# Performance work log

Hardware: AMD Instinct MI355X
Metric: run time of the kernel (lower is better)

Reference implementation:

```python
import jax, jax.numpy as jnp
import numpy as np

D_MODEL = 512
NUM_HEADS = 8
NUM_REL_EMB = 1024


def _linear(x, w, b):
    # torch nn.Linear convention: w is [out, in]
    return x @ w.T + b


def setup_inputs() -> dict:
    key = jax.random.key(0)
    B, S, D = 1, 512, D_MODEL
    ks = jax.random.split(key, 14)
    scale = D ** -0.5
    def w(i):
        return jax.random.normal(ks[i], (D, D), jnp.float32) * scale
    def b(i):
        return jax.random.normal(ks[i], (D,), jnp.float32) * 0.01
    return {
        "hidden_states": jax.random.normal(ks[0], (B, S, D), jnp.float32),
        "emb_table": jax.random.normal(ks[1], (NUM_REL_EMB, D), jnp.float32) * 0.02,
        "wq": w(2), "bq": b(3),
        "wk": w(4), "bk": b(5),
        "wv": w(6), "bv": b(7),
        "wrk": w(8), "brk": b(9),
        "wrq": w(10), "brq": b(11),
        "wo": w(12), "bo": b(13),
    }


def reference(hidden_states, emb_table, wq, bq, wk, bk, wv, bv,
              wrk, brk, wrq, brq, wo, bo):
    B, S, D = hidden_states.shape
    H = NUM_HEADS
    hd = D // H
    NE = emb_table.shape[0]

    # relative positions j - i, shifted and clamped, then embedded: [S, S, D]
    rel_pos = jnp.arange(S)[None, :] - jnp.arange(S)[:, None]
    idx = jnp.clip(rel_pos + NE // 2, 0, NE - 1)
    rel_emb = emb_table[idx]  # [S, S, D] (identical across batch)

    q = _linear(hidden_states, wq, bq).reshape(B, S, H, hd).transpose(0, 2, 1, 3)  # [B,H,S,hd]
    k = _linear(hidden_states, wk, bk).reshape(B, S, H, hd).transpose(0, 2, 1, 3)
    v = _linear(hidden_states, wv, bv).reshape(B, S, H, hd).transpose(0, 2, 1, 3)

    rk = _linear(rel_emb, wrk, brk).reshape(S, S, H, hd)  # [i, j, H, hd]
    rq = _linear(rel_emb, wrq, brq).reshape(S, S, H, hd)

    # content-content + content-relative + relative-content scores: [B,H,S,S]
    scores = (
        jnp.einsum('bhid,bhjd->bhij', q, k)
        + jnp.einsum('bhid,ijhd->bhij', q, rk)
        + jnp.einsum('ijhd,bhjd->bhij', rq, k)
    )

    attn = jax.nn.softmax(scores / jnp.sqrt(jnp.asarray(hd, scores.dtype)), axis=-1)
    # dropout is identity (p=0.0 / eval mode)

    ctx = jnp.einsum('bhij,bhjd->bhid', attn, v)          # [B,H,S,hd]
    ctx = ctx.transpose(0, 2, 1, 3).reshape(B, S, D)       # merge heads
    out = _linear(ctx, wo, bo)
    return out, attn
```

## Files before the change

kernel.cpp:

```cpp
#include <hip/hip_runtime.h>
#include <stdint.h>


typedef __bf16 bf16_t;
typedef bf16_t bf16x8 __attribute__((ext_vector_type(8)));
typedef float f32x4 __attribute__((ext_vector_type(4)));

__device__ __forceinline__ uint16_t f2bf(float f) {
  union { float f; uint32_t i; } c; c.f = f;
  return (uint16_t)((c.i + 0x7fffu + ((c.i >> 16) & 1u)) >> 16);
}
__device__ __forceinline__ uint32_t pack2bf(float lo, float hi) {
  return (uint32_t)f2bf(lo) | ((uint32_t)f2bf(hi) << 16);
}
#define MFMA(a, b, c) __builtin_amdgcn_mfma_f32_16x16x32_bf16((a), (b), (c), 0, 0, 0)

#define LSTR 40
#define SSTR 72

__global__ __launch_bounds__(256) void gemm_bt_kernel(
    const void* __restrict__ A, int lda, int zsA, int aF32,
    const void* __restrict__ B, int ldb, int zsB, int bF32,
    const float* __restrict__ bias, int hasBias,
    float* __restrict__ C, int ldc, int zsC, int K)
{
  __shared__ __align__(16) uint16_t As[64 * LSTR];
  __shared__ __align__(16) uint16_t Bs[64 * LSTR];
  const int z = blockIdx.z;
  const int m0 = blockIdx.y * 64, n0 = blockIdx.x * 64;
  const int t = threadIdx.x, lane = t & 63, wave = t >> 6;
  const int wi = wave & 1, wj = wave >> 1;
  const int quad = lane >> 4, l15 = lane & 15;
  const int srow = t >> 2, scol = (t & 3) * 8;

  f32x4 acc[2][2] = {};
  for (int k0 = 0; k0 < K; k0 += 32) {
    uint4 ap, bp;
    if (aF32) {
      const float* Af = (const float*)A + (size_t)z * zsA + (size_t)(m0 + srow) * lda + (k0 + scol);
      float4 x0 = *(const float4*)(Af); float4 x1 = *(const float4*)(Af + 4);
      ap.x = pack2bf(x0.x, x0.y); ap.y = pack2bf(x0.z, x0.w);
      ap.z = pack2bf(x1.x, x1.y); ap.w = pack2bf(x1.z, x1.w);
    } else {
      ap = *(const uint4*)((const uint16_t*)A + (size_t)z * zsA + (size_t)(m0 + srow) * lda + (k0 + scol));
    }
    if (bF32) {
      const float* Bf = (const float*)B + (size_t)z * zsB + (size_t)(n0 + srow) * ldb + (k0 + scol);
      float4 x0 = *(const float4*)(Bf); float4 x1 = *(const float4*)(Bf + 4);
      bp.x = pack2bf(x0.x, x0.y); bp.y = pack2bf(x0.z, x0.w);
      bp.z = pack2bf(x1.x, x1.y); bp.w = pack2bf(x1.z, x1.w);
    } else {
      bp = *(const uint4*)((const uint16_t*)B + (size_t)z * zsB + (size_t)(n0 + srow) * ldb + (k0 + scol));
    }
    *(uint4*)(&As[srow * LSTR + scol]) = ap;
    *(uint4*)(&Bs[srow * LSTR + scol]) = bp;
    __syncthreads();
    bf16x8 af[2], bfr[2];
#pragma unroll
    for (int x = 0; x < 2; x++) {
      af[x]  = *(const bf16x8*)(&As[(wi * 32 + x * 16 + l15) * LSTR + quad * 8]);
      bfr[x] = *(const bf16x8*)(&Bs[(wj * 32 + x * 16 + l15) * LSTR + quad * 8]);
    }
#pragma unroll
    for (int x = 0; x < 2; x++)
#pragma unroll
      for (int y = 0; y < 2; y++)
        acc[x][y] = MFMA(af[x], bfr[y], acc[x][y]);
    __syncthreads();
  }
#pragma unroll
  for (int x = 0; x < 2; x++)
#pragma unroll
    for (int y = 0; y < 2; y++) {
      const int j = n0 + wj * 32 + y * 16 + l15;
      const float bval = hasBias ? bias[j] : 0.0f;
      const int ib = m0 + wi * 32 + x * 16 + quad * 4;
#pragma unroll
      for (int r = 0; r < 4; r++)
        C[(size_t)z * zsC + (size_t)(ib + r) * ldc + j] = acc[x][y][r] + bval;
    }
}

__global__ __launch_bounds__(256) void proj_kernel(
    const float* __restrict__ X, const float* __restrict__ emb,
    const float* __restrict__ wq, const float* __restrict__ bq,
    const float* __restrict__ wk, const float* __restrict__ bk,
    const float* __restrict__ wv, const float* __restrict__ bv,
    const float* __restrict__ wrk, const float* __restrict__ brk,
    const float* __restrict__ wrq, const float* __restrict__ brq,
    uint16_t* __restrict__ q, uint16_t* __restrict__ k, uint16_t* __restrict__ vT,
    uint16_t* __restrict__ rkE, uint16_t* __restrict__ rqE)
{
  int bid = blockIdx.x;
  const float *A, *B, *bias; uint16_t* C; int mode;
  if (bid < 64)       {            A = X;   B = wq;  bias = bq;  C = q;   mode = 2; }
  else if (bid < 128) { bid -= 64; A = X;   B = wk;  bias = bk;  C = k;   mode = 2; }
  else if (bid < 192) { bid -= 128; A = X;  B = wv;  bias = bv;  C = vT;  mode = 3; }
  else if (bid < 320) { bid -= 192; A = emb; B = wrk; bias = brk; C = rkE; mode = 1; }
  else                { bid -= 320; A = emb; B = wrq; bias = brq; C = rqE; mode = 1; }
  const int m0 = (bid >> 3) * 64, n0 = (bid & 7) * 64;

  __shared__ __align__(16) uint16_t As[64 * LSTR];
  __shared__ __align__(16) uint16_t Bs[64 * LSTR];
  const int t = threadIdx.x, lane = t & 63, wave = t >> 6;
  const int wi = wave & 1, wj = wave >> 1;
  const int quad = lane >> 4, l15 = lane & 15;
  const int srow = t >> 2, scol = (t & 3) * 8;

  f32x4 acc[2][2] = {};
  for (int k0 = 0; k0 < 512; k0 += 32) {
    const float* Af = A + (size_t)(m0 + srow) * 512 + (k0 + scol);
    const float* Bf = B + (size_t)(n0 + srow) * 512 + (k0 + scol);
    float4 a0 = *(const float4*)(Af), a1 = *(const float4*)(Af + 4);
    float4 b0 = *(const float4*)(Bf), b1 = *(const float4*)(Bf + 4);
    uint4 ap, bp;
    ap.x = pack2bf(a0.x, a0.y); ap.y = pack2bf(a0.z, a0.w);
    ap.z = pack2bf(a1.x, a1.y); ap.w = pack2bf(a1.z, a1.w);
    bp.x = pack2bf(b0.x, b0.y); bp.y = pack2bf(b0.z, b0.w);
    bp.z = pack2bf(b1.x, b1.y); bp.w = pack2bf(b1.z, b1.w);
    *(uint4*)(&As[srow * LSTR + scol]) = ap;
    *(uint4*)(&Bs[srow * LSTR + scol]) = bp;
    __syncthreads();
    bf16x8 af[2], bfr[2];
#pragma unroll
    for (int x = 0; x < 2; x++) {
      af[x]  = *(const bf16x8*)(&As[(wi * 32 + x * 16 + l15) * LSTR + quad * 8]);
      bfr[x] = *(const bf16x8*)(&Bs[(wj * 32 + x * 16 + l15) * LSTR + quad * 8]);
    }
#pragma unroll
    for (int x = 0; x < 2; x++)
#pragma unroll
      for (int y = 0; y < 2; y++)
        acc[x][y] = MFMA(af[x], bfr[y], acc[x][y]);
    __syncthreads();
  }
#pragma unroll
  for (int x = 0; x < 2; x++)
#pragma unroll
    for (int y = 0; y < 2; y++) {
      const int j = n0 + wj * 32 + y * 16 + l15;
      const float bval = bias[j];
      const int ib = m0 + wi * 32 + x * 16 + quad * 4;
#pragma unroll
      for (int r = 0; r < 4; r++) {
        const int i = ib + r;
        size_t off;
        if (mode == 1)      off = (size_t)i * 512 + j;
        else if (mode == 2) off = (size_t)(j >> 6) * 32768 + (size_t)i * 64 + (size_t)(j & 63);
        else                off = (size_t)(j >> 6) * 32768 + (size_t)(j & 63) * 512 + (size_t)i;
        C[off] = f2bf(acc[x][y][r] + bval);
      }
    }
}

__global__ __launch_bounds__(256, 1) void attn_fused_kernel(
    const uint16_t* __restrict__ q, const uint16_t* __restrict__ k,
    const uint16_t* __restrict__ rkE, const uint16_t* __restrict__ rqE,
    const uint16_t* __restrict__ vT,
    float* __restrict__ attn, uint16_t* __restrict__ ctx_bf)
{
  __shared__ __align__(16) char smem[131840];
  const int h = blockIdx.y, i0 = blockIdx.x * 16;
  const int t = threadIdx.x, lane = t & 63, w = t >> 6;
  const int quad = lane >> 4, l15 = lane & 15;

  uint16_t* stgw = (uint16_t*)smem + w * 16128;
  float* U2f  = (float*)stgw;
  float* U3f  = (float*)((char*)stgw + 5376);
  uint16_t* Pw = stgw;
  float* ctxw = (float*)((char*)stgw + 8192);
  uint16_t* qs = (uint16_t*)(smem + 129024);
  float* rmax = (float*)(smem + 131328);
  float* rsum = rmax + 64;

  if (t < 128) {
    const int row = t >> 3, col = (t & 7) * 8;
    *(uint4*)(&qs[row * SSTR + col]) =
        *(const uint4*)(q + (size_t)h * 32768 + (size_t)(i0 + row) * 64 + col);
  }

  f32x4 sc[2][4];
  const int jbase = w * 2;
#pragma unroll
  for (int jt2 = 0; jt2 < 2; jt2++) {
    const int j0 = (jbase + jt2) * 64;
    const int ebase = j0 - i0 + 497;
    __syncthreads();
#pragma unroll
    for (int c = 0; c < 28; c++) {
      const int idx = lane + c * 64;
      const int row = idx >> 3, col = (idx & 7) * 8;
      const uint16_t* src;
      if (row < 64)       src = k   + (size_t)h * 32768 + (size_t)(j0 + row) * 64 + col;
      else if (row < 144) src = rqE + (size_t)min(ebase + row - 64, 1023) * 512 + h * 64 + col;
      else                src = rkE + (size_t)min(ebase + row - 144, 1023) * 512 + h * 64 + col;
      *(uint4*)(&stgw[row * SSTR + col]) = *(const uint4*)src;
    }
    __syncthreads();

    f32x4 acc1[4] = {}, acc2[5] = {}, acc3[5][4] = {};
#pragma unroll
    for (int s = 0; s < 2; s++) {
      const int ko = s * 32 + quad * 8;
      bf16x8 aq = *(const bf16x8*)(&qs[l15 * SSTR + ko]);
      bf16x8 bk[4], arq[5], brk[5];
#pragma unroll
      for (int tt = 0; tt < 4; tt++) bk[tt]  = *(const bf16x8*)(&stgw[(tt * 16 + l15) * SSTR + ko]);
#pragma unroll
      for (int x = 0; x < 5; x++)    arq[x]  = *(const bf16x8*)(&stgw[(64 + x * 16 + l15) * SSTR + ko]);
#pragma unroll
      for (int x = 0; x < 5; x++)    brk[x]  = *(const bf16x8*)(&stgw[(144 + x * 16 + l15) * SSTR + ko]);
#pragma unroll
      for (int tt = 0; tt < 4; tt++) acc1[tt] = MFMA(aq, bk[tt], acc1[tt]);
#pragma unroll
      for (int x = 0; x < 5; x++)    acc2[x] = MFMA(aq, brk[x], acc2[x]);
#pragma unroll
      for (int x = 0; x < 5; x++)
#pragma unroll
        for (int tt = 0; tt < 4; tt++) acc3[x][tt] = MFMA(arq[x], bk[tt], acc3[x][tt]);
    }
    __syncthreads();
#pragma unroll
    for (int x = 0; x < 5; x++)
#pragma unroll
      for (int r = 0; r < 4; r++)
        U2f[(quad * 4 + r) * 84 + x * 16 + l15] = acc2[x][r];
#pragma unroll
    for (int x = 0; x < 5; x++)
#pragma unroll
      for (int tt = 0; tt < 4; tt++)
#pragma unroll
        for (int r = 0; r < 4; r++)
          U3f[(x * 16 + quad * 4 + r) * 68 + tt * 16 + l15] = acc3[x][tt][r];
    __syncthreads();
#pragma unroll
    for (int tt = 0; tt < 4; tt++)
#pragma unroll
      for (int r = 0; r < 4; r++) {
        const int ii = quad * 4 + r, jj = tt * 16 + l15;
        const int rb = jj - ii + 15;
        sc[jt2][tt][r] = (acc1[tt][r] + U2f[ii * 84 + rb] + U3f[rb * 68 + jj]) * 0.125f;
      }
  }

  float mrow[4], srow[4];
#pragma unroll
  for (int r = 0; r < 4; r++) {
    float m = -1e30f;
#pragma unroll
    for (int jt2 = 0; jt2 < 2; jt2++)
#pragma unroll
      for (int tt = 0; tt < 4; tt++) m = fmaxf(m, sc[jt2][tt][r]);
#pragma unroll
    for (int o = 1; o < 16; o <<= 1) m = fmaxf(m, __shfl_xor(m, o, 64));
    mrow[r] = m;
  }
  if (l15 == 0)
#pragma unroll
    for (int r = 0; r < 4; r++) rmax[w * 16 + quad * 4 + r] = mrow[r];
  __syncthreads();
#pragma unroll
  for (int r = 0; r < 4; r++) {
    const int row = quad * 4 + r;
    const float m = fmaxf(fmaxf(rmax[row], rmax[16 + row]), fmaxf(rmax[32 + row], rmax[48 + row]));
    float s = 0.f;
#pragma unroll
    for (int jt2 = 0; jt2 < 2; jt2++)
#pragma unroll
      for (int tt = 0; tt < 4; tt++) {
        const float p = __expf(sc[jt2][tt][r] - m);
        sc[jt2][tt][r] = p; s += p;
      }
#pragma unroll
    for (int o = 1; o < 16; o <<= 1) s += __shfl_xor(s, o, 64);
    srow[r] = s;
  }
  if (l15 == 0)
#pragma unroll
    for (int r = 0; r < 4; r++) rsum[w * 16 + quad * 4 + r] = srow[r];
  __syncthreads();
#pragma unroll
  for (int r = 0; r < 4; r++) {
    const int row = quad * 4 + r;
    const float inv = 1.0f / (rsum[row] + rsum[16 + row] + rsum[32 + row] + rsum[48 + row]);
#pragma unroll
    for (int jt2 = 0; jt2 < 2; jt2++)
#pragma unroll
      for (int tt = 0; tt < 4; tt++) {
        sc[jt2][tt][r] *= inv;
        attn[((size_t)h * 512 + i0 + row) * 512 + (jbase + jt2) * 64 + tt * 16 + l15]
            = sc[jt2][tt][r];
      }
  }

  f32x4 apv[4] = {};
#pragma unroll
  for (int jt2 = 0; jt2 < 2; jt2++) {
    __syncthreads();
#pragma unroll
    for (int tt = 0; tt < 4; tt++)
#pragma unroll
      for (int r = 0; r < 4; r++)
        Pw[(quad * 4 + r) * SSTR + tt * 16 + l15] = f2bf(sc[jt2][tt][r]);
    __syncthreads();
#pragma unroll
    for (int s = 0; s < 2; s++) {
      const int ko = s * 32 + quad * 8;
      bf16x8 aP = *(const bf16x8*)(&Pw[l15 * SSTR + ko]);
#pragma unroll
      for (int tt = 0; tt < 4; tt++) {
        bf16x8 bv = *(const bf16x8*)(vT + (size_t)h * 32768 + (size_t)(tt * 16 + l15) * 512
                                     + (jbase + jt2) * 64 + ko);
        apv[tt] = MFMA(aP, bv, apv[tt]);
      }
    }
  }
#pragma unroll
  for (int tt = 0; tt < 4; tt++)
#pragma unroll
    for (int r = 0; r < 4; r++)
      ctxw[(quad * 4 + r) * 64 + tt * 16 + l15] = apv[tt][r];
  __syncthreads();
  {
    const int row = t >> 4, col = (t & 15) * 4;
    const size_t off = (size_t)(row * 64 + col) * 4;
    float4 s0 = *(const float4*)(smem + 0 * 32256 + 8192 + off);
    float4 s1 = *(const float4*)(smem + 1 * 32256 + 8192 + off);
    float4 s2 = *(const float4*)(smem + 2 * 32256 + 8192 + off);
    float4 s3 = *(const float4*)(smem + 3 * 32256 + 8192 + off);
    const float c0 = s0.x + s1.x + s2.x + s3.x;
    const float c1 = s0.y + s1.y + s2.y + s3.y;
    const float c2 = s0.z + s1.z + s2.z + s3.z;
    const float c3 = s0.w + s1.w + s2.w + s3.w;
    uint2 pk; pk.x = pack2bf(c0, c1); pk.y = pack2bf(c2, c3);
    *(uint2*)(ctx_bf + (size_t)(i0 + row) * 512 + h * 64 + col) = pk;
  }
}

extern "C" void kernel_launch(void* const* d_in, const int* in_sizes, int n_in,
                              void* d_out, int out_size, void* d_ws, size_t ws_size,
                              hipStream_t stream) {
  const float* X   = (const float*)d_in[0];
  const float* emb = (const float*)d_in[1];
  const float* wq  = (const float*)d_in[2];
  const float* bq  = (const float*)d_in[3];
  const float* wk  = (const float*)d_in[4];
  const float* bk  = (const float*)d_in[5];
  const float* wv  = (const float*)d_in[6];
  const float* bv  = (const float*)d_in[7];
  const float* wrk = (const float*)d_in[8];
  const float* brk = (const float*)d_in[9];
  const float* wrq = (const float*)d_in[10];
  const float* brq = (const float*)d_in[11];
  const float* wo  = (const float*)d_in[12];
  const float* bo  = (const float*)d_in[13];

  uint16_t* q      = (uint16_t*)d_ws;
  uint16_t* k      = q   + 262144;
  uint16_t* vT     = k   + 262144;
  uint16_t* rkE    = vT  + 262144;
  uint16_t* rqE    = rkE + 524288;
  uint16_t* ctx_bf = rqE + 524288;

  float* outp = (float*)d_out;
  float* attn = (float*)d_out + 262144;

  const dim3 blk(256);
  proj_kernel<<<dim3(448), blk, 0, stream>>>(X, emb, wq, bq, wk, bk, wv, bv,
                                             wrk, brk, wrq, brq, q, k, vT, rkE, rqE);
  attn_fused_kernel<<<dim3(32, 8), blk, 0, stream>>>(q, k, rkE, rqE, vT, attn, ctx_bf);
  gemm_bt_kernel<<<dim3(8, 8, 1), blk, 0, stream>>>(ctx_bf, 512, 0, 0,
                                                    wo, 512, 0, 1,
                                                    bo, 1, outp, 512, 0, 512);
}
```

Baseline: 131.0 us.

## Restructure attention to 8 waves per block and prefetch GEMM tiles

```diff
diff --git a/kernel.cpp b/kernel.cpp
--- a/kernel.cpp
+++ b/kernel.cpp
@@ -17,69 +17,7 @@
 
 #define LSTR 40
 #define SSTR 72
-
-__global__ __launch_bounds__(256) void gemm_bt_kernel(
-    const void* __restrict__ A, int lda, int zsA, int aF32,
-    const void* __restrict__ B, int ldb, int zsB, int bF32,
-    const float* __restrict__ bias, int hasBias,
-    float* __restrict__ C, int ldc, int zsC, int K)
-{
-  __shared__ __align__(16) uint16_t As[64 * LSTR];
-  __shared__ __align__(16) uint16_t Bs[64 * LSTR];
-  const int z = blockIdx.z;
-  const int m0 = blockIdx.y * 64, n0 = blockIdx.x * 64;
-  const int t = threadIdx.x, lane = t & 63, wave = t >> 6;
-  const int wi = wave & 1, wj = wave >> 1;
-  const int quad = lane >> 4, l15 = lane & 15;
-  const int srow = t >> 2, scol = (t & 3) * 8;
-
-  f32x4 acc[2][2] = {};
-  for (int k0 = 0; k0 < K; k0 += 32) {
-    uint4 ap, bp;
-    if (aF32) {
-      const float* Af = (const float*)A + (size_t)z * zsA + (size_t)(m0 + srow) * lda + (k0 + scol);
-      float4 x0 = *(const float4*)(Af); float4 x1 = *(const float4*)(Af + 4);
-      ap.x = pack2bf(x0.x, x0.y); ap.y = pack2bf(x0.z, x0.w);
-      ap.z = pack2bf(x1.x, x1.y); ap.w = pack2bf(x1.z, x1.w);
-    } else {
-      ap = *(const uint4*)((const uint16_t*)A + (size_t)z * zsA + (size_t)(m0 + srow) * lda + (k0 + scol));
-    }
-    if (bF32) {
-      const float* Bf = (const float*)B + (size_t)z * zsB + (size_t)(n0 + srow) * ldb + (k0 + scol);
-      float4 x0 = *(const float4*)(Bf); float4 x1 = *(const float4*)(Bf + 4);
-      bp.x = pack2bf(x0.x, x0.y); bp.y = pack2bf(x0.z, x0.w);
-      bp.z = pack2bf(x1.x, x1.y); bp.w = pack2bf(x1.z, x1.w);
-    } else {
-      bp = *(const uint4*)((const uint16_t*)B + (size_t)z * zsB + (size_t)(n0 + srow) * ldb + (k0 + scol));
-    }
-    *(uint4*)(&As[srow * LSTR + scol]) = ap;
-    *(uint4*)(&Bs[srow * LSTR + scol]) = bp;
-    __syncthreads();
-    bf16x8 af[2], bfr[2];
-#pragma unroll
-    for (int x = 0; x < 2; x++) {
-      af[x]  = *(const bf16x8*)(&As[(wi * 32 + x * 16 + l15) * LSTR + quad * 8]);
-      bfr[x] = *(const bf16x8*)(&Bs[(wj * 32 + x * 16 + l15) * LSTR + quad * 8]);
-    }
-#pragma unroll
-    for (int x = 0; x < 2; x++)
-#pragma unroll
-      for (int y = 0; y < 2; y++)
-        acc[x][y] = MFMA(af[x], bfr[y], acc[x][y]);
-    __syncthreads();
-  }
-#pragma unroll
-  for (int x = 0; x < 2; x++)
-#pragma unroll
-    for (int y = 0; y < 2; y++) {
-      const int j = n0 + wj * 32 + y * 16 + l15;
-      const float bval = hasBias ? bias[j] : 0.0f;
-      const int ib = m0 + wi * 32 + x * 16 + quad * 4;
-#pragma unroll
-      for (int r = 0; r < 4; r++)
-        C[(size_t)z * zsC + (size_t)(ib + r) * ldc + j] = acc[x][y][r] + bval;
-    }
-}
+#define RGN  13568
 
 __global__ __launch_bounds__(256) void proj_kernel(
     const float* __restrict__ X, const float* __restrict__ emb,
@@ -107,20 +45,26 @@
   const int quad = lane >> 4, l15 = lane & 15;
   const int srow = t >> 2, scol = (t & 3) * 8;
 
+  const float* Af = A + (size_t)(m0 + srow) * 512 + scol;
+  const float* Bf = B + (size_t)(n0 + srow) * 512 + scol;
+  float4 a0 = *(const float4*)(Af), a1 = *(const float4*)(Af + 4);
+  float4 b0 = *(const float4*)(Bf), b1 = *(const float4*)(Bf + 4);
+
   f32x4 acc[2][2] = {};
   for (int k0 = 0; k0 < 512; k0 += 32) {
-    const float* Af = A + (size_t)(m0 + srow) * 512 + (k0 + scol);
-    const float* Bf = B + (size_t)(n0 + srow) * 512 + (k0 + scol);
-    float4 a0 = *(const float4*)(Af), a1 = *(const float4*)(Af + 4);
-    float4 b0 = *(const float4*)(Bf), b1 = *(const float4*)(Bf + 4);
     uint4 ap, bp;
     ap.x = pack2bf(a0.x, a0.y); ap.y = pack2bf(a0.z, a0.w);
     ap.z = pack2bf(a1.x, a1.y); ap.w = pack2bf(a1.z, a1.w);
     bp.x = pack2bf(b0.x, b0.y); bp.y = pack2bf(b0.z, b0.w);
     bp.z = pack2bf(b1.x, b1.y); bp.w = pack2bf(b1.z, b1.w);
+    __syncthreads();
     *(uint4*)(&As[srow * LSTR + scol]) = ap;
     *(uint4*)(&Bs[srow * LSTR + scol]) = bp;
     __syncthreads();
+    if (k0 < 480) {
+      a0 = *(const float4*)(Af + k0 + 32); a1 = *(const float4*)(Af + k0 + 36);
+      b0 = *(const float4*)(Bf + k0 + 32); b1 = *(const float4*)(Bf + k0 + 36);
+    }
     bf16x8 af[2], bfr[2];
 #pragma unroll
     for (int x = 0; x < 2; x++) {
@@ -132,7 +76,6 @@
 #pragma unroll
       for (int y = 0; y < 2; y++)
         acc[x][y] = MFMA(af[x], bfr[y], acc[x][y]);
-    __syncthreads();
   }
 #pragma unroll
   for (int x = 0; x < 2; x++)
@@ -153,104 +96,83 @@
     }
 }
 
-__global__ __launch_bounds__(256, 1) void attn_fused_kernel(
+__global__ __launch_bounds__(512, 2) void attn_kernel(
     const uint16_t* __restrict__ q, const uint16_t* __restrict__ k,
     const uint16_t* __restrict__ rkE, const uint16_t* __restrict__ rqE,
     const uint16_t* __restrict__ vT,
     float* __restrict__ attn, uint16_t* __restrict__ ctx_bf)
 {
-  __shared__ __align__(16) char smem[131840];
+  __shared__ __align__(16) char smem[8 * RGN + 1024];
   const int h = blockIdx.y, i0 = blockIdx.x * 16;
   const int t = threadIdx.x, lane = t & 63, w = t >> 6;
   const int quad = lane >> 4, l15 = lane & 15;
-
-  uint16_t* stgw = (uint16_t*)smem + w * 16128;
-  float* U2f  = (float*)stgw;
-  float* U3f  = (float*)((char*)stgw + 5376);
-  uint16_t* Pw = stgw;
-  float* ctxw = (float*)((char*)stgw + 8192);
-  uint16_t* qs = (uint16_t*)(smem + 129024);
-  float* rmax = (float*)(smem + 131328);
-  float* rsum = rmax + 64;
-
-  if (t < 128) {
-    const int row = t >> 3, col = (t & 7) * 8;
-    *(uint4*)(&qs[row * SSTR + col]) =
-        *(const uint4*)(q + (size_t)h * 32768 + (size_t)(i0 + row) * 64 + col);
-  }
-
-  f32x4 sc[2][4];
-  const int jbase = w * 2;
-#pragma unroll
-  for (int jt2 = 0; jt2 < 2; jt2++) {
-    const int j0 = (jbase + jt2) * 64;
-    const int ebase = j0 - i0 + 497;
-    __syncthreads();
-#pragma unroll
-    for (int c = 0; c < 28; c++) {
-      const int idx = lane + c * 64;
-      const int row = idx >> 3, col = (idx & 7) * 8;
-      const uint16_t* src;
-      if (row < 64)       src = k   + (size_t)h * 32768 + (size_t)(j0 + row) * 64 + col;
-      else if (row < 144) src = rqE + (size_t)min(ebase + row - 64, 1023) * 512 + h * 64 + col;
-      else                src = rkE + (size_t)min(ebase + row - 144, 1023) * 512 + h * 64 + col;
-      *(uint4*)(&stgw[row * SSTR + col]) = *(const uint4*)src;
-    }
-    __syncthreads();
-
-    f32x4 acc1[4] = {}, acc2[5] = {}, acc3[5][4] = {};
-#pragma unroll
-    for (int s = 0; s < 2; s++) {
-      const int ko = s * 32 + quad * 8;
-      bf16x8 aq = *(const bf16x8*)(&qs[l15 * SSTR + ko]);
-      bf16x8 bk[4], arq[5], brk[5];
-#pragma unroll
-      for (int tt = 0; tt < 4; tt++) bk[tt]  = *(const bf16x8*)(&stgw[(tt * 16 + l15) * SSTR + ko]);
-#pragma unroll
-      for (int x = 0; x < 5; x++)    arq[x]  = *(const bf16x8*)(&stgw[(64 + x * 16 + l15) * SSTR + ko]);
-#pragma unroll
-      for (int x = 0; x < 5; x++)    brk[x]  = *(const bf16x8*)(&stgw[(144 + x * 16 + l15) * SSTR + ko]);
-#pragma unroll
-      for (int tt = 0; tt < 4; tt++) acc1[tt] = MFMA(aq, bk[tt], acc1[tt]);
-#pragma unroll
-      for (int x = 0; x < 5; x++)    acc2[x] = MFMA(aq, brk[x], acc2[x]);
-#pragma unroll
-      for (int x = 0; x < 5; x++)
-#pragma unroll
-        for (int tt = 0; tt < 4; tt++) acc3[x][tt] = MFMA(arq[x], bk[tt], acc3[x][tt]);
-    }
-    __syncthreads();
+  const int j0 = w * 64;
+  const int ebase = j0 - i0 + 497;
+
+  char* rgn = smem + w * RGN;
+  _Float16* U2h = (_Float16*)rgn;
+  _Float16* U3h = (_Float16*)(rgn + 2688);
+  uint16_t* Pw  = (uint16_t*)rgn;
+  float*    ctxw = (float*)(rgn + 4096);
+  float* rmax = (float*)(smem + 8 * RGN);
+  float* rsum = rmax + 128;
+
+  const uint16_t* qh = q  + (size_t)h * 32768;
+  const uint16_t* kh = k  + (size_t)h * 32768;
+  const uint16_t* vh = vT + (size_t)h * 32768;
+
+  f32x4 acc1[4] = {}, acc2[5] = {}, acc3[5][4] = {};
+#pragma unroll
+  for (int s = 0; s < 2; s++) {
+    const int ko = s * 32 + quad * 8;
+    bf16x8 aq = *(const bf16x8*)(qh + (size_t)(i0 + l15) * 64 + ko);
+    bf16x8 bk[4], arq[5], brk[5];
+#pragma unroll
+    for (int tt = 0; tt < 4; tt++)
+      bk[tt] = *(const bf16x8*)(kh + (size_t)(j0 + tt * 16 + l15) * 64 + ko);
+#pragma unroll
+    for (int x = 0; x < 5; x++) {
+      const int e = min(ebase + x * 16 + l15, 1023);
+      arq[x] = *(const bf16x8*)(rqE + (size_t)e * 512 + h * 64 + ko);
+      brk[x] = *(const bf16x8*)(rkE + (size_t)e * 512 + h * 64 + ko);
+    }
+#pragma unroll
+    for (int tt = 0; tt < 4; tt++) acc1[tt] = MFMA(aq, bk[tt], acc1[tt]);
+#pragma unroll
+    for (int x = 0; x < 5; x++)    acc2[x] = MFMA(aq, brk[x], acc2[x]);
 #pragma unroll
     for (int x = 0; x < 5; x++)
 #pragma unroll
+      for (int tt = 0; tt < 4; tt++) acc3[x][tt] = MFMA(arq[x], bk[tt], acc3[x][tt]);
+  }
+#pragma unroll
+  for (int x = 0; x < 5; x++)
+#pragma unroll
+    for (int r = 0; r < 4; r++)
+      U2h[(quad * 4 + r) * 84 + x * 16 + l15] = (_Float16)acc2[x][r];
+#pragma unroll
+  for (int x = 0; x < 5; x++)
+#pragma unroll
+    for (int tt = 0; tt < 4; tt++)
+#pragma unroll
       for (int r = 0; r < 4; r++)
-        U2f[(quad * 4 + r) * 84 + x * 16 + l15] = acc2[x][r];
-#pragma unroll
-    for (int x = 0; x < 5; x++)
-#pragma unroll
-      for (int tt = 0; tt < 4; tt++)
-#pragma unroll
-        for (int r = 0; r < 4; r++)
-          U3f[(x * 16 + quad * 4 + r) * 68 + tt * 16 + l15] = acc3[x][tt][r];
-    __syncthreads();
-#pragma unroll
-    for (int tt = 0; tt < 4; tt++)
-#pragma unroll
-      for (int r = 0; r < 4; r++) {
-        const int ii = quad * 4 + r, jj = tt * 16 + l15;
-        const int rb = jj - ii + 15;
-        sc[jt2][tt][r] = (acc1[tt][r] + U2f[ii * 84 + rb] + U3f[rb * 68 + jj]) * 0.125f;
-      }
-  }
-
-  float mrow[4], srow[4];
+        U3h[(x * 16 + quad * 4 + r) * 68 + tt * 16 + l15] = (_Float16)acc3[x][tt][r];
+  __syncthreads();
+
+  f32x4 sc[4];
+#pragma unroll
+  for (int tt = 0; tt < 4; tt++)
+#pragma unroll
+    for (int r = 0; r < 4; r++) {
+      const int ii = quad * 4 + r, jj = tt * 16 + l15;
+      const int rb = jj - ii + 15;
+      sc[tt][r] = (acc1[tt][r] + (float)U2h[ii * 84 + rb] + (float)U3h[rb * 68 + jj]) * 0.125f;
+    }
+
+  float mrow[4];
 #pragma unroll
   for (int r = 0; r < 4; r++) {
-    float m = -1e30f;
-#pragma unroll
-    for (int jt2 = 0; jt2 < 2; jt2++)
-#pragma unroll
-      for (int tt = 0; tt < 4; tt++) m = fmaxf(m, sc[jt2][tt][r]);
+    float m = fmaxf(fmaxf(sc[0][r], sc[1][r]), fmaxf(sc[2][r], sc[3][r]));
 #pragma unroll
     for (int o = 1; o < 16; o <<= 1) m = fmaxf(m, __shfl_xor(m, o, 64));
     mrow[r] = m;
@@ -259,18 +181,19 @@
 #pragma unroll
     for (int r = 0; r < 4; r++) rmax[w * 16 + quad * 4 + r] = mrow[r];
   __syncthreads();
+  float srow[4];
 #pragma unroll
   for (int r = 0; r < 4; r++) {
     const int row = quad * 4 + r;
-    const float m = fmaxf(fmaxf(rmax[row], rmax[16 + row]), fmaxf(rmax[32 + row], rmax[48 + row]));
+    float m = rmax[row];
+#pragma unroll
+    for (int x = 1; x < 8; x++) m = fmaxf(m, rmax[x * 16 + row]);
     float s = 0.f;
 #pragma unroll
-    for (int jt2 = 0; jt2 < 2; jt2++)
-#pragma unroll
-      for (int tt = 0; tt < 4; tt++) {
-        const float p = __expf(sc[jt2][tt][r] - m);
-        sc[jt2][tt][r] = p; s += p;
-      }
+    for (int tt = 0; tt < 4; tt++) {
+      const float p = __expf(sc[tt][r] - m);
+      sc[tt][r] = p; s += p;
+    }
 #pragma unroll
     for (int o = 1; o < 16; o <<= 1) s += __shfl_xor(s, o, 64);
     srow[r] = s;
@@ -282,37 +205,32 @@
 #pragma unroll
   for (int r = 0; r < 4; r++) {
     const int row = quad * 4 + r;
-    const float inv = 1.0f / (rsum[row] + rsum[16 + row] + rsum[32 + row] + rsum[48 + row]);
-#pragma unroll
-    for (int jt2 = 0; jt2 < 2; jt2++)
-#pragma unroll
-      for (int tt = 0; tt < 4; tt++) {
-        sc[jt2][tt][r] *= inv;
-        attn[((size_t)h * 512 + i0 + row) * 512 + (jbase + jt2) * 64 + tt * 16 + l15]
-            = sc[jt2][tt][r];
-      }
-  }
-
+    float s = rsum[row];
+#pragma unroll
+    for (int x = 1; x < 8; x++) s += rsum[x * 16 + row];
+    const float inv = 1.0f / s;
+#pragma unroll
+    for (int tt = 0; tt < 4; tt++) {
+      sc[tt][r] *= inv;
+      attn[((size_t)h * 512 + i0 + row) * 512 + j0 + tt * 16 + l15] = sc[tt][r];
+    }
+  }
+
+#pragma unroll
+  for (int tt = 0; tt < 4; tt++)
+#pragma unroll
+    for (int r = 0; r < 4; r++)
+      Pw[(quad * 4 + r) * SSTR + tt * 16 + l15] = f2bf(sc[tt][r]);
+  __syncthreads();
   f32x4 apv[4] = {};
 #pragma unroll
-  for (int jt2 = 0; jt2 < 2; jt2++) {
-    __syncthreads();
-#pragma unroll
-    for (int tt = 0; tt < 4; tt++)
-#pragma unroll
-      for (int r = 0; r < 4; r++)
-        Pw[(quad * 4 + r) * SSTR + tt * 16 + l15] = f2bf(sc[jt2][tt][r]);
-    __syncthreads();
-#pragma unroll
-    for (int s = 0; s < 2; s++) {
-      const int ko = s * 32 + quad * 8;
-      bf16x8 aP = *(const bf16x8*)(&Pw[l15 * SSTR + ko]);
-#pragma unroll
-      for (int tt = 0; tt < 4; tt++) {
-        bf16x8 bv = *(const bf16x8*)(vT + (size_t)h * 32768 + (size_t)(tt * 16 + l15) * 512
-                                     + (jbase + jt2) * 64 + ko);
-        apv[tt] = MFMA(aP, bv, apv[tt]);
-      }
+  for (int s = 0; s < 2; s++) {
+    const int ko = s * 32 + quad * 8;
+    bf16x8 aP = *(const bf16x8*)(&Pw[l15 * SSTR + ko]);
+#pragma unroll
+    for (int tt = 0; tt < 4; tt++) {
+      bf16x8 bv = *(const bf16x8*)(vh + (size_t)(tt * 16 + l15) * 512 + j0 + ko);
+      apv[tt] = MFMA(aP, bv, apv[tt]);
     }
   }
 #pragma unroll
@@ -322,19 +240,72 @@
       ctxw[(quad * 4 + r) * 64 + tt * 16 + l15] = apv[tt][r];
   __syncthreads();
   {
-    const int row = t >> 4, col = (t & 15) * 4;
-    const size_t off = (size_t)(row * 64 + col) * 4;
-    float4 s0 = *(const float4*)(smem + 0 * 32256 + 8192 + off);
-    float4 s1 = *(const float4*)(smem + 1 * 32256 + 8192 + off);
-    float4 s2 = *(const float4*)(smem + 2 * 32256 + 8192 + off);
-    float4 s3 = *(const float4*)(smem + 3 * 32256 + 8192 + off);
-    const float c0 = s0.x + s1.x + s2.x + s3.x;
-    const float c1 = s0.y + s1.y + s2.y + s3.y;
-    const float c2 = s0.z + s1.z + s2.z + s3.z;
-    const float c3 = s0.w + s1.w + s2.w + s3.w;
-    uint2 pk; pk.x = pack2bf(c0, c1); pk.y = pack2bf(c2, c3);
-    *(uint2*)(ctx_bf + (size_t)(i0 + row) * 512 + h * 64 + col) = pk;
-  }
+    const int idx = t * 2, row = idx >> 6, col = idx & 63;
+    const size_t off = 4096 + (size_t)(row * 64 + col) * 4;
+    float c0 = 0.f, c1 = 0.f;
+#pragma unroll
+    for (int x = 0; x < 8; x++) {
+      float2 v = *(const float2*)(smem + x * RGN + off);
+      c0 += v.x; c1 += v.y;
+    }
+    *(uint32_t*)(ctx_bf + (size_t)(i0 + row) * 512 + h * 64 + col) = pack2bf(c0, c1);
+  }
+}
+
+__global__ __launch_bounds__(256) void out_kernel(
+    const uint16_t* __restrict__ ctx_bf, const float* __restrict__ wo,
+    const float* __restrict__ bo, float* __restrict__ outp)
+{
+  __shared__ __align__(16) uint16_t As[64 * LSTR];
+  __shared__ __align__(16) uint16_t Bs[64 * LSTR];
+  const int m0 = blockIdx.y * 64, n0 = blockIdx.x * 64;
+  const int t = threadIdx.x, lane = t & 63, wave = t >> 6;
+  const int wi = wave & 1, wj = wave >> 1;
+  const int quad = lane >> 4, l15 = lane & 15;
+  const int srow = t >> 2, scol = (t & 3) * 8;
+
+  const uint16_t* Af = ctx_bf + (size_t)(m0 + srow) * 512 + scol;
+  const float* Bf = wo + (size_t)(n0 + srow) * 512 + scol;
+  uint4 ap = *(const uint4*)(Af);
+  float4 b0 = *(const float4*)(Bf), b1 = *(const float4*)(Bf + 4);
+
+  f32x4 acc[2][2] = {};
+  for (int k0 = 0; k0 < 512; k0 += 32) {
+    uint4 bp;
+    bp.x = pack2bf(b0.x, b0.y); bp.y = pack2bf(b0.z, b0.w);
+    bp.z = pack2bf(b1.x, b1.y); bp.w = pack2bf(b1.z, b1.w);
+    uint4 apc = ap;
+    __syncthreads();
+    *(uint4*)(&As[srow * LSTR + scol]) = apc;
+    *(uint4*)(&Bs[srow * LSTR + scol]) = bp;
+    __syncthreads();
+    if (k0 < 480) {
+      ap = *(const uint4*)(Af + k0 + 32);
+      b0 = *(const float4*)(Bf + k0 + 32); b1 = *(const float4*)(Bf + k0 + 36);
+    }
+    bf16x8 af[2], bfr[2];
+#pragma unroll
+    for (int x = 0; x < 2; x++) {
+      af[x]  = *(const bf16x8*)(&As[(wi * 32 + x * 16 + l15) * LSTR + quad * 8]);
+      bfr[x] = *(const bf16x8*)(&Bs[(wj * 32 + x * 16 + l15) * LSTR + quad * 8]);
+    }
+#pragma unroll
+    for (int x = 0; x < 2; x++)
+#pragma unroll
+      for (int y = 0; y < 2; y++)
+        acc[x][y] = MFMA(af[x], bfr[y], acc[x][y]);
+  }
+#pragma unroll
+  for (int x = 0; x < 2; x++)
+#pragma unroll
+    for (int y = 0; y < 2; y++) {
+      const int j = n0 + wj * 32 + y * 16 + l15;
+      const float bval = bo[j];
+      const int ib = m0 + wi * 32 + x * 16 + quad * 4;
+#pragma unroll
+      for (int r = 0; r < 4; r++)
+        outp[(size_t)(ib + r) * 512 + j] = acc[x][y][r] + bval;
+    }
 }
 
 extern "C" void kernel_launch(void* const* d_in, const int* in_sizes, int n_in,
@@ -365,11 +336,8 @@
   float* outp = (float*)d_out;
   float* attn = (float*)d_out + 262144;
 
-  const dim3 blk(256);
-  proj_kernel<<<dim3(448), blk, 0, stream>>>(X, emb, wq, bq, wk, bk, wv, bv,
-                                             wrk, brk, wrq, brq, q, k, vT, rkE, rqE);
-  attn_fused_kernel<<<dim3(32, 8), blk, 0, stream>>>(q, k, rkE, rqE, vT, attn, ctx_bf);
-  gemm_bt_kernel<<<dim3(8, 8, 1), blk, 0, stream>>>(ctx_bf, 512, 0, 0,
-                                                    wo, 512, 0, 1,
-                                                    bo, 1, outp, 512, 0, 512);
-}
+  proj_kernel<<<dim3(448), dim3(256), 0, stream>>>(X, emb, wq, bq, wk, bk, wv, bv,
+                                                   wrk, brk, wrq, brq, q, k, vT, rkE, rqE);
+  attn_kernel<<<dim3(32, 8), dim3(512), 0, stream>>>(q, k, rkE, rqE, vT, attn, ctx_bf);
+  out_kernel<<<dim3(8, 8), dim3(256), 0, stream>>>(ctx_bf, wo, bo, outp);
+}
```

Result: faster. 123.6 us (-5.7%).
